# Kernel optimization log

Hardware: AMD Instinct MI355X
Metric: run time of the kernel (lower is better)

## Reference

```python
import jax, jax.numpy as jnp
import numpy as np

# dims
B, L, IN, H, OUT = 2, 2048, 128, 512, 64
NL, ED, N, DR, K = 2, 1024, 16, 32, 4  # n_layers, d_inner=2*H, d_state, dt_rank=ceil(H/16), d_conv


def setup_inputs() -> dict:
    key = jax.random.key(0)
    ks = jax.random.split(key, 18)
    r = lambda k, s: 0.05 * jax.random.normal(k, s, dtype=jnp.float32)
    return {
        "x": jax.random.normal(ks[0], (B, L, IN), dtype=jnp.float32),
        # LiquidNet proj (in_dim -> hidden -> hidden)
        "p_Wi": r(ks[1], (IN, H)), "p_bi": r(ks[2], (H,)), "p_bh": r(ks[3], (H,)),
        "p_Wo": r(ks[4], (H, H)), "p_bo": r(ks[5], (H,)),
        # Mamba layers (stacked over layer axis)
        "m_norm_w": jnp.ones((NL, H), jnp.float32),
        "m_in_W": r(ks[6], (NL, H, 2 * ED)),
        "m_conv_w": r(ks[7], (NL, ED, K)), "m_conv_b": r(ks[8], (NL, ED)),
        "m_xproj_W": r(ks[9], (NL, ED, DR + 2 * N)),
        "m_dt_W": r(ks[10], (NL, DR, ED)), "m_dt_b": r(ks[11], (NL, ED)),
        "m_A_log": jnp.tile(jnp.log(jnp.arange(1, N + 1, dtype=jnp.float32)), (NL, ED, 1)),
        "m_D": jnp.ones((NL, ED), jnp.float32),
        "m_out_W": r(ks[12], (NL, ED, H)),
        # LiquidNet dense (hidden -> out_dim -> out_dim)
        "d_Wi": r(ks[13], (H, OUT)), "d_bi": r(ks[14], (OUT,)), "d_bh": r(ks[15], (OUT,)),
        "d_Wo": r(ks[16], (OUT, OUT)), "d_bo": r(ks[17], (OUT,)),
    }


def _rmsnorm(x, w, eps=1e-5):
    return x * jax.lax.rsqrt(jnp.mean(x * x, axis=-1, keepdims=True) + eps) * w


def _liquid(x, Wi, bi, bh, Wo, bo):
    # liquid cell with zero initial hidden state: h = tanh(i2h(x) + h2h(0))
    h = jnp.tanh(x @ Wi + bi + bh)
    return h @ Wo + bo


def _causal_conv(x, w, b):
    # x: [B, L, ED]; depthwise causal conv with kernel K
    xt = x.transpose(0, 2, 1)  # [B, ED, L]
    y = jax.lax.conv_general_dilated(xt, w[:, None, :], (1,), [(K - 1, 0)],
                                     dimension_numbers=('NCH', 'OIH', 'NCH'),
                                     feature_group_count=ED)
    return (y + b[None, :, None]).transpose(0, 2, 1)


def _ssm(xc, delta, Bm, Cm, A, D):
    # xc/delta: [B,L,ED]; Bm/Cm: [B,L,N]; A: [ED,N]; D: [ED]
    deltaA = jnp.exp(delta[..., None] * A)                              # [B,L,ED,N]
    deltaBx = delta[..., None] * Bm[:, :, None, :] * xc[..., None]      # [B,L,ED,N]

    def step(h, t):
        dA, dBx, Ct = t
        h = dA * h + dBx
        return h, jnp.einsum('bdn,bn->bd', h, Ct)

    h0 = jnp.zeros((xc.shape[0], ED, N), xc.dtype)
    _, ys = jax.lax.scan(step, h0, (deltaA.transpose(1, 0, 2, 3),
                                    deltaBx.transpose(1, 0, 2, 3),
                                    Cm.transpose(1, 0, 2)))
    return ys.transpose(1, 0, 2) + D * xc


def _mamba_block(x, norm_w, in_W, conv_w, conv_b, xproj_W, dt_W, dt_b, A_log, D, out_W):
    xn = _rmsnorm(x, norm_w)
    xz = xn @ in_W                       # [B,L,2*ED]
    xc, z = jnp.split(xz, 2, axis=-1)
    xc = jax.nn.silu(_causal_conv(xc, conv_w, conv_b))
    dbl = xc @ xproj_W                   # [B,L,DR+2N]
    dt, Bm, Cm = dbl[..., :DR], dbl[..., DR:DR + N], dbl[..., DR + N:]
    delta = jax.nn.softplus(dt @ dt_W + dt_b)
    y = _ssm(xc, delta, Bm, Cm, -jnp.exp(A_log), D)
    y = y * jax.nn.silu(z)
    return y @ out_W


def reference(x, p_Wi, p_bi, p_bh, p_Wo, p_bo,
              m_norm_w, m_in_W, m_conv_w, m_conv_b, m_xproj_W, m_dt_W, m_dt_b,
              m_A_log, m_D, m_out_W,
              d_Wi, d_bi, d_bh, d_Wo, d_bo):
    out = _liquid(x, p_Wi, p_bi, p_bh, p_Wo, p_bo)
    for l in range(NL):  # residual Mamba blocks
        out = out + _mamba_block(out, m_norm_w[l], m_in_W[l], m_conv_w[l], m_conv_b[l],
                                 m_xproj_W[l], m_dt_W[l], m_dt_b[l], m_A_log[l], m_D[l], m_out_W[l])
    out = _liquid(out, d_Wi, d_bi, d_bh, d_Wo, d_bo)
    out = out - jnp.tanh(out)  # Tanhshrink
    return out.reshape(-1)
```

## Files before the change

kernel.cpp:

```cpp
#include <hip/hip_runtime.h>
#include <hip/hip_bf16.h>
#include <cstdint>
#include <cstddef>

#define B_   2
#define L_   2048
#define IN_  128
#define H_   512
#define OUT_ 64
#define NL_  2
#define ED_  1024
#define N_   16
#define DR_  32
#define K_   4

static constexpr int M_TOK = B_ * L_;
static constexpr int SEG   = 64;
static constexpr int TS    = L_ / SEG;

typedef __attribute__((ext_vector_type(8))) short bhalf8;
typedef __attribute__((ext_vector_type(4))) float floatx4;

__device__ __forceinline__ ushort bf16bits(float f)
{
    __hip_bfloat16 h = __float2bfloat16(f);
    return *reinterpret_cast<ushort*>(&h);
}
__device__ __forceinline__ float b2f(ushort u)
{
    union { uint32_t i; float f; } x;
    x.i = ((uint32_t)u) << 16;
    return x.f;
}

__device__ __forceinline__ void gld_lds16(const ushort* g, ushort* l)
{
    __builtin_amdgcn_global_load_lds(
        (const __attribute__((address_space(1))) unsigned int*)g,
        (__attribute__((address_space(3))) unsigned int*)l, 16, 0, 0);
}

template<int BM, int BN, int BK, int EPI, bool DUAL>
__global__ __launch_bounds__(256)
void mfma_gemm(const ushort* __restrict__ A, int lda,
               const ushort* Bt, int ldb,
               const ushort* Bt2, float* C2, __hip_bfloat16* Cb2,
               const float* __restrict__ b1, const float* __restrict__ b2,
               float* C, __hip_bfloat16* Cb, int ldc,
               int M, int N, int kc)
{
    __shared__ __align__(16) ushort As[BM * BK];
    __shared__ __align__(16) ushort Bs[BN * BK];

    const int tid  = threadIdx.x;
    const int bm   = blockIdx.x * BM, bn = blockIdx.y * BN;
    int kz = 0, kbeg = 0;
    if (DUAL) {
        if (blockIdx.z) { Bt = Bt2; C = C2; Cb = Cb2; }
    } else {
        kz = blockIdx.z; kbeg = kz * kc;
    }
    const int lane = tid & 63, wave = tid >> 6;
    const int wr = wave >> 1, wc = wave & 1;
    constexpr int WM = BM / 2, WN = BN / 2;
    constexpr int FM = WM / 16, FN = WN / 16;
    const int fr = lane & 15, fg = lane >> 4;

    constexpr int ACH = BM * BK / 512;
    constexpr int BCH = BN * BK / 512;
    constexpr int RPC = 512 / BK;
    constexpr int LPR = BK / 8;
    const int sr = lane / LPR;
    const int sc = (lane % LPR) * 8;

    floatx4 acc[FM][FN] = {};

    for (int k0 = kbeg; k0 < kbeg + kc; k0 += BK) {
        #pragma unroll
        for (int i = 0; i < ACH / 4; ++i) {
            const int ci = wave * (ACH / 4) + i;
            const int r  = ci * RPC + sr;
            gld_lds16(&A[(size_t)(bm + r) * lda + k0 + sc], &As[ci * 512]);
        }
        #pragma unroll
        for (int i = 0; i < BCH / 4; ++i) {
            const int ci = wave * (BCH / 4) + i;
            const int r  = ci * RPC + sr;
            gld_lds16(&Bt[(size_t)(bn + r) * ldb + k0 + sc], &Bs[ci * 512]);
        }
        __syncthreads();
        #pragma unroll
        for (int kk = 0; kk < BK; kk += 32) {
            bhalf8 fa[FM], fb[FN];
            #pragma unroll
            for (int m = 0; m < FM; ++m)
                fa[m] = *reinterpret_cast<const bhalf8*>(
                    &As[(wr * WM + m * 16 + fr) * BK + kk + fg * 8]);
            #pragma unroll
            for (int n = 0; n < FN; ++n)
                fb[n] = *reinterpret_cast<const bhalf8*>(
                    &Bs[(wc * WN + n * 16 + fr) * BK + kk + fg * 8]);
            #pragma unroll
            for (int m = 0; m < FM; ++m)
                #pragma unroll
                for (int n = 0; n < FN; ++n)
                    acc[m][n] = __builtin_amdgcn_mfma_f32_16x16x32_bf16(
                        fa[m], fb[n], acc[m][n], 0, 0, 0);
        }
        __syncthreads();
    }

    #pragma unroll
    for (int m = 0; m < FM; ++m) {
        #pragma unroll
        for (int n = 0; n < FN; ++n) {
            const int row0 = bm + wr * WM + m * 16 + fg * 4;
            const int col  = bn + wc * WN + n * 16 + fr;
            #pragma unroll
            for (int r = 0; r < 4; ++r) {
                float v = acc[m][n][r];
                const int row = row0 + r;
                if (EPI == 0) {
                    C[(size_t)row * ldc + col] = v;
                } else if (EPI == 1) {
                    C[(size_t)row * ldc + col] += v;
                } else if (EPI == 2) {
                    Cb[(size_t)row * ldc + col] =
                        __float2bfloat16(tanhf(v + b1[col] + b2[col]));
                } else if (EPI == 3) {
                    C[(size_t)row * ldc + col] = v + b1[col];
                } else if (EPI == 4) {
                    C[(size_t)kz * M * N + (size_t)row * N + col] = v;
                } else if (EPI == 5) {
                    const float w = v + b1[col];
                    C[(size_t)row * ldc + col] = w - tanhf(w);
                } else if (EPI == 7) {
                    float* cp = C + (size_t)row * ldc + col;
                    const float w = *cp + v;
                    *cp = w;
                    Cb[(size_t)row * ldc + col] = __float2bfloat16(w);
                } else if (EPI == 8) {
                    Cb[(size_t)row * ldc + col] = __float2bfloat16(v);
                } else if (EPI == 9) {
                    const float w = v + b1[col];
                    const float sp = fmaxf(w, 0.0f) + log1pf(expf(-fabsf(w)));
                    Cb[(size_t)row * ldc + col] = __float2bfloat16(sp);
                }
            }
        }
    }
}

__global__ __launch_bounds__(256)
void xproj_gemm(const ushort* __restrict__ xcrb,
                const float* __restrict__ cw, const float* __restrict__ cb,
                const ushort* __restrict__ Bt,
                float* __restrict__ Cpart)
{
    __shared__ __align__(16) ushort As[128 * 64];
    __shared__ __align__(16) ushort Bs[64 * 64];

    const int tid = threadIdx.x;
    const int bm  = blockIdx.x * 128;
    const int kz  = blockIdx.z;
    const int lane = tid & 63, wave = tid >> 6;
    const int wr = wave >> 1, wc = wave & 1;
    const int fr = lane & 15, fg = lane >> 4;
    const int tseq0 = bm & (L_ - 1);

    const int col8 = (tid & 7) * 8;
    const int rq   = tid >> 3;
    const int sr   = lane / 8, sc2 = (lane & 7) * 8;

    floatx4 acc[4][2] = {};

    #pragma unroll
    for (int ks = 0; ks < 2; ++ks) {
        const int k0 = kz * 128 + ks * 64;

        float4 wv[8]; float cbv[8];
        #pragma unroll
        for (int j = 0; j < 8; ++j) {
            wv[j]  = *reinterpret_cast<const float4*>(&cw[(k0 + col8 + j) * 4]);
            cbv[j] = cb[k0 + col8 + j];
        }
        float xr[7][8];
        #pragma unroll
        for (int ii = 0; ii < 7; ++ii) {
            const int tok = bm + rq * 4 - 3 + ii;
            const int tokc = tok < 0 ? 0 : tok;
            const bhalf8 v = *reinterpret_cast<const bhalf8*>(
                &xcrb[(size_t)tokc * ED_ + k0 + col8]);
            #pragma unroll
            for (int j = 0; j < 8; ++j) xr[ii][j] = b2f((ushort)v[j]);
        }
        #pragma unroll
        for (int rr = 0; rr < 4; ++rr) {
            const int trow = tseq0 + rq * 4 + rr;
            __align__(16) ushort ob[8];
            #pragma unroll
            for (int j = 0; j < 8; ++j) {
                float a = cbv[j] + wv[j].w * xr[rr + 3][j];
                if (trow >= 1) a += wv[j].z * xr[rr + 2][j];
                if (trow >= 2) a += wv[j].y * xr[rr + 1][j];
                if (trow >= 3) a += wv[j].x * xr[rr + 0][j];
                const float s = a / (1.0f + __expf(-a));
                ob[j] = bf16bits(s);
            }
            *reinterpret_cast<uint4*>(&As[(rq * 4 + rr) * 64 + col8]) =
                *reinterpret_cast<const uint4*>(ob);
        }
        #pragma unroll
        for (int i = 0; i < 2; ++i) {
            const int ci = wave * 2 + i;
            const int r  = ci * 8 + sr;
            gld_lds16(&Bt[(size_t)r * ED_ + k0 + sc2], &Bs[ci * 512]);
        }
        __syncthreads();
        #pragma unroll
        for (int kk = 0; kk < 64; kk += 32) {
            bhalf8 fa[4], fb[2];
            #pragma unroll
            for (int m = 0; m < 4; ++m)
                fa[m] = *reinterpret_cast<const bhalf8*>(
                    &As[(wr * 64 + m * 16 + fr) * 64 + kk + fg * 8]);
            #pragma unroll
            for (int n = 0; n < 2; ++n)
                fb[n] = *reinterpret_cast<const bhalf8*>(
                    &Bs[(wc * 32 + n * 16 + fr) * 64 + kk + fg * 8]);
            #pragma unroll
            for (int m = 0; m < 4; ++m)
                #pragma unroll
                for (int n = 0; n < 2; ++n)
                    acc[m][n] = __builtin_amdgcn_mfma_f32_16x16x32_bf16(
                        fa[m], fb[n], acc[m][n], 0, 0, 0);
        }
        __syncthreads();
    }

    #pragma unroll
    for (int m = 0; m < 4; ++m) {
        #pragma unroll
        for (int n = 0; n < 2; ++n) {
            const int row0 = bm + wr * 64 + m * 16 + fg * 4;
            const int col  = wc * 32 + n * 16 + fr;
            #pragma unroll
            for (int r = 0; r < 4; ++r)
                Cpart[(size_t)kz * M_TOK * 64 + (size_t)(row0 + r) * 64 + col] =
                    acc[m][n][r];
        }
    }
}

template<int NP, int ACT, bool B1, bool B2, int OUTMODE>
__global__ __launch_bounds__(256)
void reduce_part_k(const float* __restrict__ P, const float* __restrict__ b1,
                   const float* __restrict__ b2, float* __restrict__ Of,
                   __hip_bfloat16* __restrict__ Ob, int MN, int Ncols)
{
    const int i = blockIdx.x * 256 + threadIdx.x;
    float s = 0.0f;
    #pragma unroll
    for (int z = 0; z < NP; ++z) s += P[(size_t)z * MN + i];
    const int col = i & (Ncols - 1);
    if (B1) s += b1[col];
    if (B2) s += b2[col];
    if (ACT == 1) s = tanhf(s);
    if (OUTMODE == 0 || OUTMODE == 2) Of[i] = s;
    if (OUTMODE == 1 || OUTMODE == 2) Ob[i] = __float2bfloat16(s);
}

__device__ __forceinline__ void tr32(float (*t)[33],
                                     const float* __restrict__ W,
                                     __hip_bfloat16* __restrict__ Wt,
                                     int K, int N, int local, int gx, int tid)
{
    const int kx = local % gx, ny = local / gx;
    const int k0 = kx * 32, n0 = ny * 32;
    const int c = tid & 31, r4 = tid >> 5;
    #pragma unroll
    for (int i = 0; i < 4; ++i) {
        const int rr = r4 + i * 8;
        t[rr][c] = W[(size_t)(k0 + rr) * N + n0 + c];
    }
    __syncthreads();
    #pragma unroll
    for (int i = 0; i < 4; ++i) {
        const int rr = r4 + i * 8;
        Wt[(size_t)(n0 + rr) * K + k0 + c] = __float2bfloat16(t[c][rr]);
    }
}

__global__ __launch_bounds__(256)
void prep_k(const float* __restrict__ x, __hip_bfloat16* __restrict__ Xb,
            const float* pWi, __hip_bfloat16* TpWi,
            const float* pWo, __hip_bfloat16* TpWo,
            const float* inW, __hip_bfloat16* TinW0, __hip_bfloat16* TinW1,
            const float* xpW, __hip_bfloat16* TxpW0, __hip_bfloat16* TxpW1,
            const float* outW, __hip_bfloat16* ToutW0, __hip_bfloat16* ToutW1,
            const float* dWi, __hip_bfloat16* TdWi,
            const float* dtW, __hip_bfloat16* TdtW0, __hip_bfloat16* TdtW1,
            const float* dWo, __hip_bfloat16* TdWo)
{
    __shared__ float t[32][33];
    const int tid = threadIdx.x;
    int r = blockIdx.x;

    if (r < 512) {
        const int i = (r * 256 + tid) * 4;
        const float4 v = *reinterpret_cast<const float4*>(&x[i]);
        ushort4 u;
        u.x = bf16bits(v.x); u.y = bf16bits(v.y);
        u.z = bf16bits(v.z); u.w = bf16bits(v.w);
        *reinterpret_cast<ushort4*>(&Xb[i]) = u;
        return;
    }
    r -= 512;
    if (r < 64)   { tr32(t, pWi, TpWi, IN_, H_, r, 4, tid); return; }   r -= 64;
    if (r < 256)  { tr32(t, pWo, TpWo, H_, H_, r, 16, tid); return; }   r -= 256;
    if (r < 1024) { tr32(t, inW, TinW0, H_, 2 * ED_, r, 16, tid); return; } r -= 1024;
    if (r < 1024) { tr32(t, inW + (size_t)H_ * 2 * ED_, TinW1, H_, 2 * ED_, r, 16, tid); return; } r -= 1024;
    if (r < 64)   { tr32(t, xpW, TxpW0, ED_, 64, r, 32, tid); return; } r -= 64;
    if (r < 64)   { tr32(t, xpW + (size_t)ED_ * 64, TxpW1, ED_, 64, r, 32, tid); return; } r -= 64;
    if (r < 512)  { tr32(t, outW, ToutW0, ED_, H_, r, 32, tid); return; } r -= 512;
    if (r < 512)  { tr32(t, outW + (size_t)ED_ * H_, ToutW1, ED_, H_, r, 32, tid); return; } r -= 512;
    if (r < 32)   { tr32(t, dWi, TdWi, H_, OUT_, r, 16, tid); return; } r -= 32;
    if (r < 32)   { tr32(t, dtW, TdtW0, DR_, ED_, r, 1, tid); return; } r -= 32;
    if (r < 32)   { tr32(t, dtW + DR_ * ED_, TdtW1, DR_, ED_, r, 1, tid); return; } r -= 32;
    tr32(t, dWo, TdWo, OUT_, OUT_, r, 2, tid);
}
static constexpr int PREP_BLOCKS = 512 + 64 + 256 + 1024 + 1024 + 64 + 64 + 512 + 512 + 32 + 32 + 32 + 4;

__global__ __launch_bounds__(256)
void rmsnorm_k(const float* __restrict__ x, const float* __restrict__ w,
               __hip_bfloat16* __restrict__ o)
{
    const int row = blockIdx.x;
    const int tid = threadIdx.x;
    const float* xr = x + (size_t)row * H_;
    float v0 = xr[tid], v1 = xr[tid + 256];
    float s = v0 * v0 + v1 * v1;
    #pragma unroll
    for (int off = 32; off > 0; off >>= 1) s += __shfl_down(s, off, 64);
    __shared__ float ps[4];
    __shared__ float scale_s;
    const int wave = tid >> 6, lane = tid & 63;
    if (lane == 0) ps[wave] = s;
    __syncthreads();
    if (tid == 0) {
        float tot = ps[0] + ps[1] + ps[2] + ps[3];
        scale_s = rsqrtf(tot * (1.0f / H_) + 1e-5f);
    }
    __syncthreads();
    const float sc = scale_s;
    o[(size_t)row * H_ + tid]       = __float2bfloat16(v0 * sc * w[tid]);
    o[(size_t)row * H_ + tid + 256] = __float2bfloat16(v1 * sc * w[tid + 256]);
}

template<bool P3>
__global__ __launch_bounds__(256)
void ssm_scan_k(const ushort* __restrict__ deltab,
                const ushort* __restrict__ xcrb,
                const float* __restrict__ dbl,
                const float* __restrict__ cw, const float* __restrict__ cb,
                const ushort* __restrict__ zb,
                const float* __restrict__ A_log,
                const float* __restrict__ Dv,
                float* __restrict__ hend, float* __restrict__ pprod,
                const float* __restrict__ hinit,
                __hip_bfloat16* __restrict__ ybuf)
{
    __shared__ float sdl[TS][64];
    __shared__ float sxc[TS][64];
    __shared__ float bc[TS][32];

    const int bx   = blockIdx.x;
    const int seg  = bx & (SEG - 1);
    const int dblk = (bx >> 6) & 15;
    const int b    = bx >> 10;
    const int tid  = threadIdx.x;
    const int dbase = dblk * 64;
    const int t0   = seg * TS;
    const size_t row0 = (size_t)(b * L_ + t0);
    const int dls = tid & 63;

    {
        const int rowt = tid >> 3;
        const int d8   = (tid & 7) * 8;
        const bhalf8 v = *reinterpret_cast<const bhalf8*>(
            &deltab[(row0 + rowt) * ED_ + dbase + d8]);
        #pragma unroll
        for (int j = 0; j < 8; ++j) sdl[rowt][d8 + j] = b2f((ushort)v[j]);
    }
    {
        const int tg = tid >> 6;
        const int tb = tg * 8;
        float xr[11];
        #pragma unroll
        for (int ii = 0; ii < 11; ++ii) {
            const int gt = t0 + tb - 3 + ii;
            xr[ii] = (gt >= 0)
                ? b2f(xcrb[((size_t)(b * L_) + gt) * ED_ + dbase + dls]) : 0.0f;
        }
        const float4 w = *reinterpret_cast<const float4*>(&cw[(dbase + dls) * 4]);
        const float cbv = cb[dbase + dls];
        #pragma unroll
        for (int k = 0; k < 8; ++k) {
            const float a = cbv + w.x * xr[k] + w.y * xr[k + 1]
                          + w.z * xr[k + 2] + w.w * xr[k + 3];
            sxc[tb + k][dls] = a / (1.0f + __expf(-a));
        }
    }
    #pragma unroll
    for (int e = 0; e < 4; ++e) {
        const int lin = tid + e * 256;
        bc[lin >> 5][lin & 31] = dbl[(row0 + (lin >> 5)) * 64 + 32 + (lin & 31)];
    }
    __syncthreads();

    const int dl = tid >> 2;
    const int ng = tid & 3;
    const int d  = dbase + dl;

    float Av[4];
    #pragma unroll
    for (int i = 0; i < 4; ++i) Av[i] = -expf(A_log[d * N_ + ng * 4 + i]);

    float h[4];
    float S = 0.0f;
    if (P3) {
        #pragma unroll
        for (int i = 0; i < 4; ++i)
            h[i] = hinit[((size_t)(b * SEG + seg) * N_ + ng * 4 + i) * ED_ + d];
    } else {
        #pragma unroll
        for (int i = 0; i < 4; ++i) h[i] = 0.0f;
    }
    const float Dd = P3 ? Dv[d] : 0.0f;

    #pragma unroll
    for (int t = 0; t < TS; ++t) {
        const float dvt = sdl[t][dl];
        const float xvt = sxc[t][dl];
        const float dx  = dvt * xvt;
        if (!P3) S += dvt;
        float ysum = 0.0f;
        #pragma unroll
        for (int i = 0; i < 4; ++i) {
            const float dA = __expf(dvt * Av[i]);
            h[i] = fmaf(dA, h[i], dx * bc[t][ng * 4 + i]);
            if (P3) ysum = fmaf(h[i], bc[t][16 + ng * 4 + i], ysum);
        }
        if (P3) {
            float y2 = ysum + __shfl_xor(ysum, 1, 64);
            float y4 = y2 + __shfl_xor(y2, 2, 64);
            if (ng == 0) {
                const float zv = b2f(zb[(row0 + t) * ED_ + d]);
                const float sz = zv / (1.0f + __expf(-zv));
                ybuf[(row0 + t) * ED_ + d] =
                    __float2bfloat16((y4 + Dd * xvt) * sz);
            }
        }
    }

    if (!P3) {
        #pragma unroll
        for (int i = 0; i < 4; ++i) {
            const size_t o = ((size_t)(b * SEG + seg) * N_ + ng * 4 + i) * ED_ + d;
            hend[o]  = h[i];
            pprod[o] = __expf(Av[i] * S);
        }
    }
}

__global__ __launch_bounds__(256)
void ssm_combine_k(const float* __restrict__ hend, const float* __restrict__ pprod,
                   float* __restrict__ hinit)
{
    const int gid = blockIdx.x * 256 + threadIdx.x;
    const int d = gid & (ED_ - 1);
    const int n = (gid >> 10) & (N_ - 1);
    const int b = gid >> 14;
    size_t o = ((size_t)(b * SEG) * N_ + n) * ED_ + d;
    const size_t stride = (size_t)N_ * ED_;
    float h = 0.0f;
    #pragma unroll 8
    for (int s = 0; s < SEG; ++s) {
        hinit[o] = h;
        h = fmaf(pprod[o], h, hend[o]);
        o += stride;
    }
}

extern "C" void kernel_launch(void* const* d_in, const int* in_sizes, int n_in,
                              void* d_out, int out_size, void* d_ws, size_t ws_size,
                              hipStream_t stream)
{
    const float* x      = (const float*)d_in[0];
    const float* p_Wi   = (const float*)d_in[1];
    const float* p_bi   = (const float*)d_in[2];
    const float* p_bh   = (const float*)d_in[3];
    const float* p_Wo   = (const float*)d_in[4];
    const float* p_bo   = (const float*)d_in[5];
    const float* m_norm = (const float*)d_in[6];
    const float* m_inW  = (const float*)d_in[7];
    const float* m_cw   = (const float*)d_in[8];
    const float* m_cb   = (const float*)d_in[9];
    const float* m_xpW  = (const float*)d_in[10];
    const float* m_dtW  = (const float*)d_in[11];
    const float* m_dtb  = (const float*)d_in[12];
    const float* m_Alog = (const float*)d_in[13];
    const float* m_D    = (const float*)d_in[14];
    const float* m_outW = (const float*)d_in[15];
    const float* d_Wi   = (const float*)d_in[16];
    const float* d_bi   = (const float*)d_in[17];
    const float* d_bh   = (const float*)d_in[18];
    const float* d_Wo   = (const float*)d_in[19];
    const float* d_bo   = (const float*)d_in[20];
    float* out_f = (float*)d_out;
    float* ws = (float*)d_ws;

    float* OUT   = ws;
    float* XCRB  = ws + 2097152;
    float* ZB    = ws + 4194304;
    float* DELB  = ws + 6291456;
    float* HEND  = ws + 8388608;
    float* PPROD = ws + 10485760;
    float* HINIT = ws + 12582912;
    float* BF    = ws + 14680064;
    float* WT    = ws + 16777216;
    float* DBL   = ws + 18630656;
    float* DBLF  = ws + 18892800;

    float* CPARTX = HEND;
    float* CPART2 = XCRB;
    __hip_bfloat16* Xb    = (__hip_bfloat16*)BF;
    __hip_bfloat16* H1b   = (__hip_bfloat16*)(BF + 262144);
    __hip_bfloat16* XNb   = (__hip_bfloat16*)BF;
    __hip_bfloat16* YB    = (__hip_bfloat16*)BF;
    __hip_bfloat16* H2b   = (__hip_bfloat16*)DBL;
    __hip_bfloat16* OUTb  = (__hip_bfloat16*)PPROD;
    __hip_bfloat16* DBLb  = (__hip_bfloat16*)DBLF;
    __hip_bfloat16* XCRbp = (__hip_bfloat16*)XCRB;
    __hip_bfloat16* Zbp   = (__hip_bfloat16*)ZB;
    __hip_bfloat16* DELbp = (__hip_bfloat16*)DELB;

    __hip_bfloat16* WTu     = (__hip_bfloat16*)WT;
    __hip_bfloat16* T_pWi   = WTu;
    __hip_bfloat16* T_pWo   = WTu + 65536;
    __hip_bfloat16* T_inW0  = WTu + 327680;
    __hip_bfloat16* T_inW1  = WTu + 1376256;
    __hip_bfloat16* T_xpW0  = WTu + 2424832;
    __hip_bfloat16* T_xpW1  = WTu + 2490368;
    __hip_bfloat16* T_outW0 = WTu + 2555904;
    __hip_bfloat16* T_outW1 = WTu + 3080192;
    __hip_bfloat16* T_dWi   = WTu + 3604480;
    __hip_bfloat16* T_dtW0  = WTu + 3637248;
    __hip_bfloat16* T_dtW1  = WTu + 3670016;
    __hip_bfloat16* T_dWo   = WTu + 3702784;

    const dim3 blk(256);

    prep_k<<<dim3(PREP_BLOCKS), blk, 0, stream>>>(
        x, Xb, p_Wi, T_pWi, p_Wo, T_pWo, m_inW, T_inW0, T_inW1,
        m_xpW, T_xpW0, T_xpW1, m_outW, T_outW0, T_outW1,
        d_Wi, T_dWi, m_dtW, T_dtW0, T_dtW1, d_Wo, T_dWo);

    mfma_gemm<128, 64, 64, 2, false><<<dim3(32, 8), blk, 0, stream>>>(
        (const ushort*)Xb, IN_, (const ushort*)T_pWi, IN_,
        nullptr, nullptr, nullptr,
        p_bi, p_bh, nullptr, H1b, H_, M_TOK, H_, IN_);
    mfma_gemm<128, 64, 64, 3, false><<<dim3(32, 8), blk, 0, stream>>>(
        (const ushort*)H1b, H_, (const ushort*)T_pWo, H_,
        nullptr, nullptr, nullptr,
        p_bo, nullptr, OUT, nullptr, H_, M_TOK, H_, H_);

    for (int l = 0; l < NL_; ++l) {
        const float* nw   = m_norm + l * H_;
        const float* cw   = m_cw   + l * ED_ * K_;
        const float* cb   = m_cb   + l * ED_;
        const float* dtb  = m_dtb  + l * ED_;
        const float* Alog = m_Alog + l * ED_ * N_;
        const float* Dv   = m_D    + l * ED_;
        const __hip_bfloat16* TinW  = l ? T_inW1  : T_inW0;
        const __hip_bfloat16* TxpW  = l ? T_xpW1  : T_xpW0;
        const __hip_bfloat16* ToutW = l ? T_outW1 : T_outW0;
        const __hip_bfloat16* TdtW  = l ? T_dtW1  : T_dtW0;

        rmsnorm_k<<<dim3(M_TOK), blk, 0, stream>>>(OUT, nw, XNb);
        mfma_gemm<128, 128, 64, 8, true><<<dim3(32, 8, 2), blk, 0, stream>>>(
            (const ushort*)XNb, H_, (const ushort*)TinW, H_,
            (const ushort*)(TinW + (size_t)ED_ * H_), nullptr, Zbp,
            nullptr, nullptr, nullptr, XCRbp, ED_, M_TOK, ED_, H_);
        xproj_gemm<<<dim3(32, 1, 8), blk, 0, stream>>>(
            (const ushort*)XCRbp, cw, cb, (const ushort*)TxpW, CPARTX);
        reduce_part_k<8, 0, false, false, 2><<<dim3(1024), blk, 0, stream>>>(
            CPARTX, nullptr, nullptr, DBL, DBLb, M_TOK * 64, 64);
        mfma_gemm<128, 64, 32, 9, false><<<dim3(32, 16), blk, 0, stream>>>(
            (const ushort*)DBLb, 64, (const ushort*)TdtW, DR_,
            nullptr, nullptr, nullptr,
            dtb, nullptr, nullptr, DELbp, ED_, M_TOK, ED_, DR_);
        ssm_scan_k<false><<<dim3(2048), blk, 0, stream>>>(
            (const ushort*)DELbp, (const ushort*)XCRbp, DBL, cw, cb,
            nullptr, Alog, nullptr, HEND, PPROD, nullptr, nullptr);
        ssm_combine_k<<<dim3(128), blk, 0, stream>>>(HEND, PPROD, HINIT);
        ssm_scan_k<true><<<dim3(2048), blk, 0, stream>>>(
            (const ushort*)DELbp, (const ushort*)XCRbp, DBL, cw, cb,
            (const ushort*)Zbp, Alog, Dv, nullptr, nullptr, HINIT, YB);
        if (l == 0) {
            mfma_gemm<128, 64, 64, 1, false><<<dim3(32, 8), blk, 0, stream>>>(
                (const ushort*)YB, ED_, (const ushort*)ToutW, ED_,
                nullptr, nullptr, nullptr,
                nullptr, nullptr, OUT, nullptr, H_, M_TOK, H_, ED_);
        } else {
            mfma_gemm<128, 64, 64, 7, false><<<dim3(32, 8), blk, 0, stream>>>(
                (const ushort*)YB, ED_, (const ushort*)ToutW, ED_,
                nullptr, nullptr, nullptr,
                nullptr, nullptr, OUT, OUTb, H_, M_TOK, H_, ED_);
        }
    }

    mfma_gemm<128, 64, 64, 4, false><<<dim3(32, 1, 8), blk, 0, stream>>>(
        (const ushort*)OUTb, H_, (const ushort*)T_dWi, H_,
        nullptr, nullptr, nullptr,
        nullptr, nullptr, CPART2, nullptr, 64, M_TOK, 64, H_ / 8);
    reduce_part_k<8, 1, true, true, 1><<<dim3(1024), blk, 0, stream>>>(
        CPART2, d_bi, d_bh, nullptr, H2b, M_TOK * 64, 64);
    mfma_gemm<128, 64, 64, 5, false><<<dim3(32, 1), blk, 0, stream>>>(
        (const ushort*)H2b, OUT_, (const ushort*)T_dWo, OUT_,
        nullptr, nullptr, nullptr,
        d_bo, nullptr, out_f, nullptr, OUT_, M_TOK, OUT_, OUT_);
}
```

Before: 321.1 us.

## Fuse output head, store SSM carries in bf16, widen GEMM tiles

Replaces the split-K head GEMM, reduction and second small GEMM with one fused kernel that computes tanh(xWi+b) in shared memory and applies Wo plus Tanhshrink directly. The SSM chunk scan now writes only the per-segment delta sum instead of a full per-state decay product, and the combine recomputes the decay and writes initial states in bf16, cutting intermediate traffic. Several H-wide GEMMs switch to 128x128 tiles with half the grid. The final out-projection no longer writes the fp32 residual back, only the bf16 copy. Bf16 hinit adds rounding error, and the larger tiles launch fewer blocks.

```diff
diff --git a/kernel.cpp b/kernel.cpp
--- a/kernel.cpp
+++ b/kernel.cpp
@@ -131,20 +131,15 @@
                     C[(size_t)row * ldc + col] = v + b1[col];
                 } else if (EPI == 4) {
                     C[(size_t)kz * M * N + (size_t)row * N + col] = v;
-                } else if (EPI == 5) {
-                    const float w = v + b1[col];
-                    C[(size_t)row * ldc + col] = w - tanhf(w);
-                } else if (EPI == 7) {
-                    float* cp = C + (size_t)row * ldc + col;
-                    const float w = *cp + v;
-                    *cp = w;
-                    Cb[(size_t)row * ldc + col] = __float2bfloat16(w);
                 } else if (EPI == 8) {
                     Cb[(size_t)row * ldc + col] = __float2bfloat16(v);
                 } else if (EPI == 9) {
                     const float w = v + b1[col];
                     const float sp = fmaxf(w, 0.0f) + log1pf(expf(-fabsf(w)));
                     Cb[(size_t)row * ldc + col] = __float2bfloat16(sp);
+                } else if (EPI == 10) {
+                    const float w = C[(size_t)row * ldc + col] + v;
+                    Cb[(size_t)row * ldc + col] = __float2bfloat16(w);
                 }
             }
         }
@@ -268,6 +263,98 @@
     if (ACT == 1) s = tanhf(s);
     if (OUTMODE == 0 || OUTMODE == 2) Of[i] = s;
     if (OUTMODE == 1 || OUTMODE == 2) Ob[i] = __float2bfloat16(s);
+}
+
+__global__ __launch_bounds__(256)
+void head_fused_k(const ushort* __restrict__ Ab,
+                  const ushort* __restrict__ Wi,
+                  const ushort* __restrict__ Wo,
+                  const float* __restrict__ bi, const float* __restrict__ bh,
+                  const float* __restrict__ bo,
+                  float* __restrict__ out)
+{
+    __shared__ __align__(16) ushort As[32 * 64];
+    __shared__ __align__(16) ushort Bs[64 * 64];
+    __shared__ __align__(16) ushort Hs[32 * 64];
+    __shared__ __align__(16) ushort Ws[64 * 64];
+
+    const int tid = threadIdx.x;
+    const int bm = blockIdx.x * 32;
+    const int lane = tid & 63, wave = tid >> 6;
+    const int wr = wave >> 1, wc = wave & 1;
+    const int fr = lane & 15, fg = lane >> 4;
+    const int sr = lane / 8, sc = (lane & 7) * 8;
+
+    #pragma unroll
+    for (int i = 0; i < 2; ++i) {
+        const int ci = wave * 2 + i;
+        const int r = ci * 8 + sr;
+        gld_lds16(&Wo[(size_t)r * 64 + sc], &Ws[ci * 512]);
+    }
+
+    floatx4 acc[2] = {};
+    for (int k0 = 0; k0 < 512; k0 += 64) {
+        {
+            const int r = wave * 8 + sr;
+            gld_lds16(&Ab[(size_t)(bm + r) * 512 + k0 + sc], &As[wave * 512]);
+        }
+        #pragma unroll
+        for (int i = 0; i < 2; ++i) {
+            const int ci = wave * 2 + i;
+            const int r = ci * 8 + sr;
+            gld_lds16(&Wi[(size_t)r * 512 + k0 + sc], &Bs[ci * 512]);
+        }
+        __syncthreads();
+        #pragma unroll
+        for (int kk = 0; kk < 64; kk += 32) {
+            const bhalf8 fa = *reinterpret_cast<const bhalf8*>(
+                &As[(wr * 16 + fr) * 64 + kk + fg * 8]);
+            #pragma unroll
+            for (int n = 0; n < 2; ++n) {
+                const bhalf8 fb = *reinterpret_cast<const bhalf8*>(
+                    &Bs[(wc * 32 + n * 16 + fr) * 64 + kk + fg * 8]);
+                acc[n] = __builtin_amdgcn_mfma_f32_16x16x32_bf16(
+                    fa, fb, acc[n], 0, 0, 0);
+            }
+        }
+        __syncthreads();
+    }
+    #pragma unroll
+    for (int n = 0; n < 2; ++n) {
+        const int col = wc * 32 + n * 16 + fr;
+        const float bb = bi[col] + bh[col];
+        #pragma unroll
+        for (int r = 0; r < 4; ++r) {
+            const int row = wr * 16 + fg * 4 + r;
+            Hs[row * 64 + col] = bf16bits(tanhf(acc[n][r] + bb));
+        }
+    }
+    __syncthreads();
+
+    floatx4 acc2[2] = {};
+    #pragma unroll
+    for (int kk = 0; kk < 64; kk += 32) {
+        const bhalf8 fa = *reinterpret_cast<const bhalf8*>(
+            &Hs[(wr * 16 + fr) * 64 + kk + fg * 8]);
+        #pragma unroll
+        for (int n = 0; n < 2; ++n) {
+            const bhalf8 fb = *reinterpret_cast<const bhalf8*>(
+                &Ws[(wc * 32 + n * 16 + fr) * 64 + kk + fg * 8]);
+            acc2[n] = __builtin_amdgcn_mfma_f32_16x16x32_bf16(
+                fa, fb, acc2[n], 0, 0, 0);
+        }
+    }
+    #pragma unroll
+    for (int n = 0; n < 2; ++n) {
+        const int col = wc * 32 + n * 16 + fr;
+        const float bb = bo[col];
+        #pragma unroll
+        for (int r = 0; r < 4; ++r) {
+            const int row = wr * 16 + fg * 4 + r;
+            const float w = acc2[n][r] + bb;
+            out[(size_t)(bm + row) * 64 + col] = w - tanhf(w);
+        }
+    }
 }
 
 __device__ __forceinline__ void tr32(float (*t)[33],
@@ -366,8 +453,8 @@
                 const ushort* __restrict__ zb,
                 const float* __restrict__ A_log,
                 const float* __restrict__ Dv,
-                float* __restrict__ hend, float* __restrict__ pprod,
-                const float* __restrict__ hinit,
+                float* __restrict__ hend, float* __restrict__ Sbuf,
+                const ushort* __restrict__ hinitb,
                 __hip_bfloat16* __restrict__ ybuf)
 {
     __shared__ float sdl[TS][64];
@@ -431,7 +518,7 @@
     if (P3) {
         #pragma unroll
         for (int i = 0; i < 4; ++i)
-            h[i] = hinit[((size_t)(b * SEG + seg) * N_ + ng * 4 + i) * ED_ + d];
+            h[i] = b2f(hinitb[((size_t)(b * SEG + seg) * N_ + ng * 4 + i) * ED_ + d]);
     } else {
         #pragma unroll
         for (int i = 0; i < 4; ++i) h[i] = 0.0f;
@@ -465,30 +552,33 @@
 
     if (!P3) {
         #pragma unroll
-        for (int i = 0; i < 4; ++i) {
-            const size_t o = ((size_t)(b * SEG + seg) * N_ + ng * 4 + i) * ED_ + d;
-            hend[o]  = h[i];
-            pprod[o] = __expf(Av[i] * S);
-        }
+        for (int i = 0; i < 4; ++i)
+            hend[((size_t)(b * SEG + seg) * N_ + ng * 4 + i) * ED_ + d] = h[i];
+        if (ng == 0)
+            Sbuf[(size_t)(b * SEG + seg) * ED_ + d] = S;
     }
 }
 
 __global__ __launch_bounds__(256)
-void ssm_combine_k(const float* __restrict__ hend, const float* __restrict__ pprod,
-                   float* __restrict__ hinit)
+void ssm_combine_k(const float* __restrict__ hend, const float* __restrict__ Sbuf,
+                   const float* __restrict__ A_log,
+                   __hip_bfloat16* __restrict__ hinitb)
 {
     const int gid = blockIdx.x * 256 + threadIdx.x;
     const int d = gid & (ED_ - 1);
     const int n = (gid >> 10) & (N_ - 1);
     const int b = gid >> 14;
-    size_t o = ((size_t)(b * SEG) * N_ + n) * ED_ + d;
+    const float Av = -expf(A_log[d * N_ + n]);
+    size_t o  = ((size_t)(b * SEG) * N_ + n) * ED_ + d;
+    size_t so = (size_t)(b * SEG) * ED_ + d;
     const size_t stride = (size_t)N_ * ED_;
     float h = 0.0f;
-    #pragma unroll 8
+    #pragma unroll 4
     for (int s = 0; s < SEG; ++s) {
-        hinit[o] = h;
-        h = fmaf(pprod[o], h, hend[o]);
+        hinitb[o] = __float2bfloat16(h);
+        h = fmaf(__expf(Av * Sbuf[so]), h, hend[o]);
         o += stride;
+        so += ED_;
     }
 }
 
@@ -520,27 +610,27 @@
     float* out_f = (float*)d_out;
     float* ws = (float*)d_ws;
 
-    float* OUT   = ws;
-    float* XCRB  = ws + 2097152;
-    float* ZB    = ws + 4194304;
-    float* DELB  = ws + 6291456;
-    float* HEND  = ws + 8388608;
-    float* PPROD = ws + 10485760;
-    float* HINIT = ws + 12582912;
-    float* BF    = ws + 14680064;
-    float* WT    = ws + 16777216;
-    float* DBL   = ws + 18630656;
-    float* DBLF  = ws + 18892800;
+    float* OUT    = ws;
+    float* XCRB   = ws + 2097152;
+    float* ZB     = ws + 4194304;
+    float* DELB   = ws + 6291456;
+    float* HEND   = ws + 8388608;
+    float* OUTBR  = ws + 10485760;
+    float* HINITB = ws + 11534336;
+    float* BF     = ws + 12582912;
+    float* WT     = ws + 14680064;
+    float* DBL    = ws + 16533504;
+    float* DBLF   = ws + 16795648;
 
     float* CPARTX = HEND;
-    float* CPART2 = XCRB;
+    float* SBUF   = DBLF;
     __hip_bfloat16* Xb    = (__hip_bfloat16*)BF;
     __hip_bfloat16* H1b   = (__hip_bfloat16*)(BF + 262144);
     __hip_bfloat16* XNb   = (__hip_bfloat16*)BF;
     __hip_bfloat16* YB    = (__hip_bfloat16*)BF;
-    __hip_bfloat16* H2b   = (__hip_bfloat16*)DBL;
-    __hip_bfloat16* OUTb  = (__hip_bfloat16*)PPROD;
+    __hip_bfloat16* OUTb  = (__hip_bfloat16*)OUTBR;
     __hip_bfloat16* DBLb  = (__hip_bfloat16*)DBLF;
+    __hip_bfloat16* HINb  = (__hip_bfloat16*)HINITB;
     __hip_bfloat16* XCRbp = (__hip_bfloat16*)XCRB;
     __hip_bfloat16* Zbp   = (__hip_bfloat16*)ZB;
     __hip_bfloat16* DELbp = (__hip_bfloat16*)DELB;
@@ -566,11 +656,11 @@
         m_xpW, T_xpW0, T_xpW1, m_outW, T_outW0, T_outW1,
         d_Wi, T_dWi, m_dtW, T_dtW0, T_dtW1, d_Wo, T_dWo);
 
-    mfma_gemm<128, 64, 64, 2, false><<<dim3(32, 8), blk, 0, stream>>>(
+    mfma_gemm<128, 128, 64, 2, false><<<dim3(32, 4), blk, 0, stream>>>(
         (const ushort*)Xb, IN_, (const ushort*)T_pWi, IN_,
         nullptr, nullptr, nullptr,
         p_bi, p_bh, nullptr, H1b, H_, M_TOK, H_, IN_);
-    mfma_gemm<128, 64, 64, 3, false><<<dim3(32, 8), blk, 0, stream>>>(
+    mfma_gemm<128, 128, 64, 3, false><<<dim3(32, 4), blk, 0, stream>>>(
         (const ushort*)H1b, H_, (const ushort*)T_pWo, H_,
         nullptr, nullptr, nullptr,
         p_bo, nullptr, OUT, nullptr, H_, M_TOK, H_, H_);
@@ -602,32 +692,26 @@
             dtb, nullptr, nullptr, DELbp, ED_, M_TOK, ED_, DR_);
         ssm_scan_k<false><<<dim3(2048), blk, 0, stream>>>(
             (const ushort*)DELbp, (const ushort*)XCRbp, DBL, cw, cb,
-            nullptr, Alog, nullptr, HEND, PPROD, nullptr, nullptr);
-        ssm_combine_k<<<dim3(128), blk, 0, stream>>>(HEND, PPROD, HINIT);
+            nullptr, Alog, nullptr, HEND, SBUF, nullptr, nullptr);
+        ssm_combine_k<<<dim3(128), blk, 0, stream>>>(HEND, SBUF, Alog, HINb);
         ssm_scan_k<true><<<dim3(2048), blk, 0, stream>>>(
             (const ushort*)DELbp, (const ushort*)XCRbp, DBL, cw, cb,
-            (const ushort*)Zbp, Alog, Dv, nullptr, nullptr, HINIT, YB);
+            (const ushort*)Zbp, Alog, Dv, nullptr, nullptr,
+            (const ushort*)HINb, YB);
         if (l == 0) {
-            mfma_gemm<128, 64, 64, 1, false><<<dim3(32, 8), blk, 0, stream>>>(
+            mfma_gemm<128, 128, 64, 1, false><<<dim3(32, 4), blk, 0, stream>>>(
                 (const ushort*)YB, ED_, (const ushort*)ToutW, ED_,
                 nullptr, nullptr, nullptr,
                 nullptr, nullptr, OUT, nullptr, H_, M_TOK, H_, ED_);
         } else {
-            mfma_gemm<128, 64, 64, 7, false><<<dim3(32, 8), blk, 0, stream>>>(
+            mfma_gemm<128, 128, 64, 10, false><<<dim3(32, 4), blk, 0, stream>>>(
                 (const ushort*)YB, ED_, (const ushort*)ToutW, ED_,
                 nullptr, nullptr, nullptr,
                 nullptr, nullptr, OUT, OUTb, H_, M_TOK, H_, ED_);
         }
     }
 
-    mfma_gemm<128, 64, 64, 4, false><<<dim3(32, 1, 8), blk, 0, stream>>>(
-        (const ushort*)OUTb, H_, (const ushort*)T_dWi, H_,
-        nullptr, nullptr, nullptr,
-        nullptr, nullptr, CPART2, nullptr, 64, M_TOK, 64, H_ / 8);
-    reduce_part_k<8, 1, true, true, 1><<<dim3(1024), blk, 0, stream>>>(
-        CPART2, d_bi, d_bh, nullptr, H2b, M_TOK * 64, 64);
-    mfma_gemm<128, 64, 64, 5, false><<<dim3(32, 1), blk, 0, stream>>>(
-        (const ushort*)H2b, OUT_, (const ushort*)T_dWo, OUT_,
-        nullptr, nullptr, nullptr,
-        d_bo, nullptr, out_f, nullptr, OUT_, M_TOK, OUT_, OUT_);
-}
+    head_fused_k<<<dim3(M_TOK / 32), blk, 0, stream>>>(
+        (const ushort*)OUTb, (const ushort*)T_dWi, (const ushort*)T_dWo,
+        d_bi, d_bh, d_bo, out_f);
+}
```

Measured after the change: 350.1 us. 9.0% more time.
